# Kernel tuning notes

Measured on AMD Instinct MI355X. Metric: run time of the kernel, lower is better.

The kernel has to match this reference:

```python
import jax, jax.numpy as jnp
import numpy as np

HIDDEN = 128

def setup_inputs() -> dict:
    key = jax.random.key(0)
    ks = jax.random.split(key, 12)
    N, T, H = 4096, 64, HIDDEN
    s_in = 1.0 / np.sqrt(2.0)
    s_h = 1.0 / np.sqrt(H)
    return {
        "x_seq": jax.random.normal(ks[0], (N, T), dtype=jnp.float32),
        "m_seq": jax.random.uniform(ks[1], (N, T), dtype=jnp.float32),
        # linear layers stored as [in, out] (math identical to torch x @ W.T + b)
        "W_in": jax.random.normal(ks[2], (2, H), dtype=jnp.float32) * s_in,
        "b_in": jax.random.normal(ks[3], (H,), dtype=jnp.float32) * 0.01,
        "W_proj": jax.random.normal(ks[4], (H, H), dtype=jnp.float32) * s_h,
        "b_proj": jax.random.normal(ks[5], (H,), dtype=jnp.float32) * 0.01,
        "W_gcn": jax.random.normal(ks[6], (H, H), dtype=jnp.float32) * s_h,
        "b_gcn": jax.random.normal(ks[7], (H,), dtype=jnp.float32) * 0.01,
        "W_out": jax.random.normal(ks[8], (H, 1), dtype=jnp.float32) * s_h,
        "b_out": jax.random.normal(ks[9], (1,), dtype=jnp.float32) * 0.01,
    }


def reference(x_seq, m_seq, W_in, b_in, W_proj, b_proj, W_gcn, b_gcn, W_out, b_out):
    N, T = x_seq.shape
    H = W_in.shape[1]
    scale = 1.0 / jnp.sqrt(jnp.asarray(H, dtype=x_seq.dtype))
    # [T, N, 2] time-major inputs for scan
    xs = jnp.stack([x_seq, m_seq], axis=-1).transpose(1, 0, 2)
    h0 = jnp.zeros((N, H), dtype=x_seq.dtype)

    def step(h, inp_t):
        h_in = jax.nn.relu(inp_t @ W_in + b_in)            # [N, H]
        h_proj = h @ W_proj + b_proj                        # [N, H]
        A_dyn = jax.nn.softmax(h_proj @ h_proj.T * scale, axis=1)  # [N, N]
        msg = A_dyn @ h_in                                  # [N, H]
        h_new = jax.nn.relu(msg @ W_gcn + b_gcn + h_in)     # [N, H]
        pred = (h_new @ W_out + b_out)[:, 0]                # [N]
        return h_new, pred

    _, preds = jax.lax.scan(step, h0, xs)  # preds: [T, N]
    return preds.T  # [N, T]
```

## Files before the change

### kernel.cpp

```cpp
#include <hip/hip_runtime.h>
#include <math.h>

#define NN 4096
#define TT 64
#define HH 128
#define NNP 4160
#define SLICE (128 * NNP)
#define SPLITS 8
#define KPB (NN / SPLITS)
#define KT 32
#define NTILES (KPB / KT)
#define QB 64
#define SCALE 0.08838834764831845f
#define CSHIFT 16.0f

typedef __attribute__((ext_vector_type(8))) short short8;
typedef __attribute__((ext_vector_type(4))) float f32x4;
typedef unsigned long long u64;
#define MFMA(a, b, c)   __builtin_amdgcn_mfma_f32_16x16x32_bf16((a), (b), (c), 0, 0, 0)

__device__ __forceinline__ short f2b(float f) {
    union { float f; unsigned u; } v; v.f = f;
    unsigned r = v.u + 0x7fffu + ((v.u >> 16) & 1u);
    return (short)(r >> 16);
}
__device__ __forceinline__ float b2f(short s) {
    union { unsigned u; float f; } v; v.u = ((unsigned)(unsigned short)s) << 16;
    return v.f;
}
__device__ __forceinline__ void lds_fence() {
    __asm__ __volatile__("s_waitcnt lgkmcnt(0)" ::: "memory");
}


__global__ __launch_bounds__(256) void prep_kernel(
    const float* __restrict__ x_seq, const float* __restrict__ m_seq,
    const float* __restrict__ W_in,  const float* __restrict__ b_in,
    const float* __restrict__ W_proj,const float* __restrict__ b_proj,
    const float* __restrict__ W_gcn,
    short* __restrict__ hp, short* __restrict__ hinT_all,
    short* __restrict__ WgT, short* __restrict__ WpT)
{
    __shared__ __align__(16) short hb[128 * 66];
    const int b = blockIdx.x, tid = threadIdx.x;
    if (b < 256) {
        const int n0 = b * 16;
        for (int i = tid; i < 16 * HH; i += 256) {
            const int q = i >> 7, j = i & 127, n = n0 + q;
            hp[n * HH + j] = f2b(b_proj[j]);
        }
    } else if (b < 272) {
        const int wb = b - 256;
        #pragma unroll
        for (int k = 0; k < 4; ++k) {
            const int idx = wb * 1024 + k * 256 + tid;
            const int n = idx >> 7, kk = idx & 127;
            WgT[idx] = f2b(W_gcn[kk * HH + n]);
            WpT[idx] = f2b(W_proj[kk * HH + n]);
        }
    } else {
        const int u = b - 272;
        const int t = u >> 6, n0 = (u & 63) * 64;
        for (int i = tid; i < 64 * HH; i += 256) {
            const int q = i >> 7, j = i & 127, n = n0 + q;
            float hv = x_seq[n * TT + t] * W_in[j] + m_seq[n * TT + t] * W_in[HH + j] + b_in[j];
            hv = hv > 0.f ? hv : 0.f;
            hb[j * 66 + q] = f2b(hv);
        }
        __syncthreads();
        short* dst = hinT_all + (size_t)t * SLICE;
        for (int c = tid; c < 128 * 16; c += 256) {
            const int j = c >> 4, off = (c & 15) * 4;
            const int nb = n0 + off;
            const int tcol = (nb & ~31) | (((nb >> 2) & 3) << 3) | (((nb >> 4) & 1) << 2);
            const unsigned lo = *(const unsigned*)&hb[j * 66 + off];
            const unsigned hi = *(const unsigned*)&hb[j * 66 + off + 2];
            const u64 v = (u64)lo | ((u64)hi << 32);
            *(u64*)&dst[(size_t)j * NNP + tcol] = v;
        }
    }
}

__global__ __launch_bounds__(256, 3) void attn_kernel(
    const short* __restrict__ hp, const short* __restrict__ hinT,
    short* __restrict__ OpartB, float* __restrict__ lpart)
{
    __shared__ __align__(16) char pool[37888];
    short* KtS = (short*)pool;
    short* VtS = (short*)(pool + 17408);

    const int tid  = threadIdx.x;
    const int wave = tid >> 6, lane = tid & 63;
    const int ln = lane & 15, g = lane >> 4;
    const int split = blockIdx.x >> 6, qg = blockIdx.x & 63;
    const int q0 = qg * QB + wave * 16;
    const int kbase = split * KPB;

    const int krow = tid >> 4, kcol = (tid & 15) * 8;
    const int vrow = tid >> 2, vcol = (tid & 3) * 8;

    short8 qf[4];
    #pragma unroll
    for (int kc = 0; kc < 4; ++kc)
        qf[kc] = *(const short8*)&hp[(q0 + ln) * HH + kc * 32 + g * 8];

    f32x4 oacc[8] = {};
    f32x4 lacc = {};
    short8 vone;
    #pragma unroll
    for (int e = 0; e < 8; ++e) vone[e] = (short)0x3F80;

    short8 ksA0, ksA1, vsA0, vsA1;
    auto load_tile = [&](int kt_) {
        const int kb = kbase + kt_ * KT;
        ksA0 = *(const short8*)&hp  [(kb + krow) * HH + kcol];
        ksA1 = *(const short8*)&hp  [(kb + krow + 16) * HH + kcol];
        vsA0 = *(const short8*)&hinT[(size_t)vrow * NNP + kb + vcol];
        vsA1 = *(const short8*)&hinT[(size_t)(vrow + 64) * NNP + kb + vcol];
    };
    auto store_tile = [&](int b) {
        *(short8*)&KtS[b * 4352 + krow * 136 + kcol]        = ksA0;
        *(short8*)&KtS[b * 4352 + (krow + 16) * 136 + kcol] = ksA1;
        *(short8*)&VtS[b * 5120 + vrow * 40 + vcol]         = vsA0;
        *(short8*)&VtS[b * 5120 + (vrow + 64) * 40 + vcol]  = vsA1;
    };

    load_tile(0);
    store_tile(0);

    for (int kt = 0; kt < NTILES; ++kt) {
        const int b = kt & 1;
        __syncthreads();

        short8 kf[2][4], vf[8];
        #pragma unroll
        for (int kt2 = 0; kt2 < 2; ++kt2)
            #pragma unroll
            for (int kc = 0; kc < 4; ++kc)
                kf[kt2][kc] = *(const short8*)&KtS[b * 4352 + (kt2 * 16 + ln) * 136 + kc * 32 + g * 8];
        #pragma unroll
        for (int dt = 0; dt < 8; ++dt)
            vf[dt] = *(const short8*)&VtS[b * 5120 + (dt * 16 + ln) * 40 + g * 8];

        if (kt + 1 < NTILES) load_tile(kt + 1);

        f32x4 st[2] = {};
        __builtin_amdgcn_s_setprio(1);
        #pragma unroll
        for (int kt2 = 0; kt2 < 2; ++kt2)
            #pragma unroll
            for (int kc = 0; kc < 4; ++kc)
                st[kt2] = MFMA(kf[kt2][kc], qf[kc], st[kt2]);
        __builtin_amdgcn_s_setprio(0);

        short8 pa;
        #pragma unroll
        for (int e = 0; e < 8; ++e) {
            const float s = (e < 4) ? st[0][e] : st[1][e - 4];
            pa[e] = f2b(__expf(s * SCALE - CSHIFT));
        }

        if (kt + 1 < NTILES) store_tile(b ^ 1);

        __builtin_amdgcn_s_setprio(1);
        #pragma unroll
        for (int dt = 0; dt < 8; ++dt)
            oacc[dt] = MFMA(pa, vf[dt], oacc[dt]);
        lacc = MFMA(pa, vone, lacc);
        __builtin_amdgcn_s_setprio(0);
    }

    __syncthreads();

    if (ln == 0) {
        #pragma unroll
        for (int r = 0; r < 4; ++r)
            lpart[split * NN + q0 + g * 4 + r] = lacc[r];
    }

    short* bounce = (short*)pool + wave * 2048;
    #pragma unroll
    for (int dt = 0; dt < 8; ++dt)
        #pragma unroll
        for (int r = 0; r < 4; ++r)
            bounce[(g * 4 + r) * 128 + dt * 16 + ln] = f2b(oacc[dt][r]);
    lds_fence();
    #pragma unroll
    for (int sub = 0; sub < 4; ++sub) {
        const int qrow = sub * 4 + (lane >> 4), chunk = lane & 15;
        const short8 rd = *(const short8*)&bounce[qrow * 128 + chunk * 8];
        *(short8*)&OpartB[((size_t)split * NN + q0 + qrow) * HH + chunk * 8] = rd;
    }
}

__global__ __launch_bounds__(512) void fuse_kernel(
    const short* __restrict__ OpartB, const float* __restrict__ lpart,
    short* __restrict__ hp,
    const short* __restrict__ WgT, const short* __restrict__ WpT,
    const float* __restrict__ b_gcn, const float* __restrict__ b_proj,
    const float* __restrict__ W_out, const float* __restrict__ b_out,
    const float* __restrict__ x_seq, const float* __restrict__ m_seq,
    const float* __restrict__ W_in,  const float* __restrict__ b_in,
    float* __restrict__ out, int t)
{
    __shared__ __align__(16) short msgb[16 * 136];
    __shared__ __align__(16) short hnb[16 * 136];
    __shared__ float larr[16];
    __shared__ float ppd[8 * 16];

    const int tid = threadIdx.x;
    const int wave = tid >> 6, lane = tid & 63;
    const int ln = lane & 15, g = lane >> 4;
    const int fb = blockIdx.x;
    const int qg64 = (fb & 7) + 8 * (fb >> 5);
    const int qb = qg64 * 64 + ((fb >> 3) & 3) * 16;

    if (tid < 16) {
        float l = 0.f;
        #pragma unroll
        for (int sp = 0; sp < SPLITS; ++sp) l += lpart[sp * NN + qb + tid];
        larr[tid] = 1.0f / l;
    }
    __syncthreads();

    if (tid < 256) {
        const int q = tid >> 4, c8 = (tid & 15) * 8;
        float s[8] = {0.f, 0.f, 0.f, 0.f, 0.f, 0.f, 0.f, 0.f};
        #pragma unroll
        for (int sp = 0; sp < SPLITS; ++sp) {
            const short8 v = *(const short8*)&OpartB[((size_t)sp * NN + qb + q) * HH + c8];
            #pragma unroll
            for (int k = 0; k < 8; ++k) s[k] += b2f(v[k]);
        }
        const float inv = larr[q];
        short* mp = &msgb[q * 136 + c8];
        #pragma unroll
        for (int k = 0; k < 8; ++k) mp[k] = f2b(s[k] * inv);
    }
    __syncthreads();

    {
        short8 af[4];
        #pragma unroll
        for (int kc = 0; kc < 4; ++kc)
            af[kc] = *(const short8*)&msgb[ln * 136 + kc * 32 + g * 8];
        f32x4 c = {};
        #pragma unroll
        for (int kc = 0; kc < 4; ++kc)
            c = MFMA(af[kc], *(const short8*)&WgT[(wave * 16 + ln) * HH + kc * 32 + g * 8], c);
        const int j = wave * 16 + ln;
        const float bg = b_gcn[j], wo = W_out[j];
        const float wj0 = W_in[j], wj1 = W_in[HH + j], bj = b_in[j];
        float pr[4];
        #pragma unroll
        for (int r = 0; r < 4; ++r) {
            const int q = g * 4 + r;
            float hv = x_seq[(qb + q) * TT + t] * wj0 + m_seq[(qb + q) * TT + t] * wj1 + bj;
            hv = hv > 0.f ? hv : 0.f;
            float v = c[r] + bg + b2f(f2b(hv));
            v = v > 0.f ? v : 0.f;
            hnb[q * 136 + j] = f2b(v);
            pr[r] = v * wo;
        }
        #pragma unroll
        for (int r = 0; r < 4; ++r) {
            float p = pr[r];
            p += __shfl_xor(p, 1); p += __shfl_xor(p, 2);
            p += __shfl_xor(p, 4); p += __shfl_xor(p, 8);
            if (ln == 0) ppd[wave * 16 + g * 4 + r] = p;
        }
    }
    __syncthreads();

    if (tid < 16) {
        float s = b_out[0];
        #pragma unroll
        for (int w = 0; w < 8; ++w) s += ppd[w * 16 + tid];
        out[(qb + tid) * TT + t] = s;
    }

    if (t < TT - 1) {
        short8 hf[4];
        #pragma unroll
        for (int kc = 0; kc < 4; ++kc)
            hf[kc] = *(const short8*)&hnb[ln * 136 + kc * 32 + g * 8];
        f32x4 c = {};
        #pragma unroll
        for (int kc = 0; kc < 4; ++kc)
            c = MFMA(hf[kc], *(const short8*)&WpT[(wave * 16 + ln) * HH + kc * 32 + g * 8], c);
        const float bp = b_proj[wave * 16 + ln];
        #pragma unroll
        for (int r = 0; r < 4; ++r)
            hp[(qb + g * 4 + r) * HH + wave * 16 + ln] = f2b(c[r] + bp);
    }
}

extern "C" void kernel_launch(void* const* d_in, const int* in_sizes, int n_in,
                              void* d_out, int out_size, void* d_ws, size_t ws_size,
                              hipStream_t stream) {
    const float* x_seq  = (const float*)d_in[0];
    const float* m_seq  = (const float*)d_in[1];
    const float* W_in   = (const float*)d_in[2];
    const float* b_in   = (const float*)d_in[3];
    const float* W_proj = (const float*)d_in[4];
    const float* b_proj = (const float*)d_in[5];
    const float* W_gcn  = (const float*)d_in[6];
    const float* b_gcn  = (const float*)d_in[7];
    const float* W_out  = (const float*)d_in[8];
    const float* b_out  = (const float*)d_in[9];
    float* out = (float*)d_out;

    char* base = (char*)d_ws;
    const size_t MB = 1 << 20;
    short* hp       = (short*)(base + 0 * MB);
    short* WgT      = (short*)(base + 3 * MB);
    short* WpT      = (short*)(base + 3 * MB + 32768);
    float* lpart    = (float*)(base + 3 * MB + 65536);
    short* OpartB   = (short*)(base + 4 * MB);
    short* hinT_all = (short*)(base + 32 * MB);

    prep_kernel<<<272 + 64 * 64, 256, 0, stream>>>(x_seq, m_seq, W_in, b_in,
                                                   W_proj, b_proj, W_gcn,
                                                   hp, hinT_all, WgT, WpT);

    for (int t = 0; t < TT; ++t) {
        const short* hinT_t = hinT_all + (size_t)t * SLICE;
        attn_kernel<<<(NN / QB) * SPLITS, 256, 0, stream>>>(hp, hinT_t, OpartB, lpart);
        fuse_kernel<<<NN / 16, 512, 0, stream>>>(OpartB, lpart, hp,
                                                 WgT, WpT, b_gcn, b_proj, W_out, b_out,
                                                 x_seq, m_seq, W_in, b_in, out, t);
    }
}
```

Before: 1.613 ms.

## Give each attention wave two query tiles and split key tiles between wave pairs

Each wave in the attention kernel now covers 32 queries (two 16-row tiles) instead of 16, so every K/V fragment read from LDS feeds twice as many MFMAs. The block's key tiles are split in halves between the two wave pairs, and the partial outputs and row sums are merged through an fp32 LDS buffer before the bf16 write-out. The intent is to cut LDS fragment traffic per MFMA. In exchange, register pressure rises (launch bounds lowered to 2 blocks), half the waves sit idle in every key-tile iteration while still hitting the barriers, and the epilogue gains an extra cross-wave reduction.

```diff
diff --git a/kernel.cpp b/kernel.cpp
--- a/kernel.cpp
+++ b/kernel.cpp
@@ -81,31 +81,36 @@
     }
 }
 
-__global__ __launch_bounds__(256, 3) void attn_kernel(
+__global__ __launch_bounds__(256, 2) void attn_kernel(
     const short* __restrict__ hp, const short* __restrict__ hinT,
     short* __restrict__ OpartB, float* __restrict__ lpart)
 {
-    __shared__ __align__(16) char pool[37888];
+    __shared__ __align__(16) char pool[38144];
     short* KtS = (short*)pool;
     short* VtS = (short*)(pool + 17408);
+    float* obuf = (float*)pool;
+    float* lbuf = (float*)(pool + 33792);
 
     const int tid  = threadIdx.x;
     const int wave = tid >> 6, lane = tid & 63;
     const int ln = lane & 15, g = lane >> 4;
     const int split = blockIdx.x >> 6, qg = blockIdx.x & 63;
-    const int q0 = qg * QB + wave * 16;
+    const int qh = wave & 1, kh = wave >> 1;
+    const int q0 = qg * QB + qh * 32;
     const int kbase = split * KPB;
 
     const int krow = tid >> 4, kcol = (tid & 15) * 8;
     const int vrow = tid >> 2, vcol = (tid & 3) * 8;
 
-    short8 qf[4];
+    short8 qf[2][4];
     #pragma unroll
-    for (int kc = 0; kc < 4; ++kc)
-        qf[kc] = *(const short8*)&hp[(q0 + ln) * HH + kc * 32 + g * 8];
-
-    f32x4 oacc[8] = {};
-    f32x4 lacc = {};
+    for (int qt = 0; qt < 2; ++qt)
+        #pragma unroll
+        for (int kc = 0; kc < 4; ++kc)
+            qf[qt][kc] = *(const short8*)&hp[(q0 + qt * 16 + ln) * HH + kc * 32 + g * 8];
+
+    f32x4 oacc[2][8] = {};
+    f32x4 lacc[2] = {};
     short8 vone;
     #pragma unroll
     for (int e = 0; e < 8; ++e) vone[e] = (short)0x3F80;
@@ -132,64 +137,105 @@
         const int b = kt & 1;
         __syncthreads();
 
+        const bool act = ((kt >> 3) == kh);
         short8 kf[2][4], vf[8];
-        #pragma unroll
-        for (int kt2 = 0; kt2 < 2; ++kt2)
-            #pragma unroll
-            for (int kc = 0; kc < 4; ++kc)
-                kf[kt2][kc] = *(const short8*)&KtS[b * 4352 + (kt2 * 16 + ln) * 136 + kc * 32 + g * 8];
-        #pragma unroll
-        for (int dt = 0; dt < 8; ++dt)
-            vf[dt] = *(const short8*)&VtS[b * 5120 + (dt * 16 + ln) * 40 + g * 8];
+        if (act) {
+            #pragma unroll
+            for (int kt2 = 0; kt2 < 2; ++kt2)
+                #pragma unroll
+                for (int kc = 0; kc < 4; ++kc)
+                    kf[kt2][kc] = *(const short8*)&KtS[b * 4352 + (kt2 * 16 + ln) * 136 + kc * 32 + g * 8];
+            #pragma unroll
+            for (int dt = 0; dt < 8; ++dt)
+                vf[dt] = *(const short8*)&VtS[b * 5120 + (dt * 16 + ln) * 40 + g * 8];
+        }
 
         if (kt + 1 < NTILES) load_tile(kt + 1);
 
-        f32x4 st[2] = {};
-        __builtin_amdgcn_s_setprio(1);
-        #pragma unroll
-        for (int kt2 = 0; kt2 < 2; ++kt2)
-            #pragma unroll
-            for (int kc = 0; kc < 4; ++kc)
-                st[kt2] = MFMA(kf[kt2][kc], qf[kc], st[kt2]);
-        __builtin_amdgcn_s_setprio(0);
-
-        short8 pa;
-        #pragma unroll
-        for (int e = 0; e < 8; ++e) {
-            const float s = (e < 4) ? st[0][e] : st[1][e - 4];
-            pa[e] = f2b(__expf(s * SCALE - CSHIFT));
+        short8 pa[2];
+        if (act) {
+            f32x4 st[2][2] = {};
+            __builtin_amdgcn_s_setprio(1);
+            #pragma unroll
+            for (int kt2 = 0; kt2 < 2; ++kt2)
+                #pragma unroll
+                for (int qt = 0; qt < 2; ++qt)
+                    #pragma unroll
+                    for (int kc = 0; kc < 4; ++kc)
+                        st[kt2][qt] = MFMA(kf[kt2][kc], qf[qt][kc], st[kt2][qt]);
+            __builtin_amdgcn_s_setprio(0);
+
+            #pragma unroll
+            for (int qt = 0; qt < 2; ++qt) {
+                short8 paq;
+                #pragma unroll
+                for (int e = 0; e < 8; ++e) {
+                    const float s = (e < 4) ? st[0][qt][e] : st[1][qt][e - 4];
+                    paq[e] = f2b(__expf(s * SCALE - CSHIFT));
+                }
+                pa[qt] = paq;
+            }
         }
 
         if (kt + 1 < NTILES) store_tile(b ^ 1);
 
-        __builtin_amdgcn_s_setprio(1);
-        #pragma unroll
-        for (int dt = 0; dt < 8; ++dt)
-            oacc[dt] = MFMA(pa, vf[dt], oacc[dt]);
-        lacc = MFMA(pa, vone, lacc);
-        __builtin_amdgcn_s_setprio(0);
-    }
-
-    __syncthreads();
-
-    if (ln == 0) {
-        #pragma unroll
-        for (int r = 0; r < 4; ++r)
-            lpart[split * NN + q0 + g * 4 + r] = lacc[r];
-    }
-
-    short* bounce = (short*)pool + wave * 2048;
-    #pragma unroll
-    for (int dt = 0; dt < 8; ++dt)
-        #pragma unroll
-        for (int r = 0; r < 4; ++r)
-            bounce[(g * 4 + r) * 128 + dt * 16 + ln] = f2b(oacc[dt][r]);
-    lds_fence();
-    #pragma unroll
-    for (int sub = 0; sub < 4; ++sub) {
-        const int qrow = sub * 4 + (lane >> 4), chunk = lane & 15;
-        const short8 rd = *(const short8*)&bounce[qrow * 128 + chunk * 8];
-        *(short8*)&OpartB[((size_t)split * NN + q0 + qrow) * HH + chunk * 8] = rd;
+        if (act) {
+            __builtin_amdgcn_s_setprio(1);
+            #pragma unroll
+            for (int qt = 0; qt < 2; ++qt) {
+                #pragma unroll
+                for (int dt = 0; dt < 8; ++dt)
+                    oacc[qt][dt] = MFMA(pa[qt], vf[dt], oacc[qt][dt]);
+                lacc[qt] = MFMA(pa[qt], vone, lacc[qt]);
+            }
+            __builtin_amdgcn_s_setprio(0);
+        }
+    }
+
+    __syncthreads();
+
+    if (kh == 0) {
+        #pragma unroll
+        for (int qt = 0; qt < 2; ++qt) {
+            #pragma unroll
+            for (int dt = 0; dt < 8; ++dt)
+                #pragma unroll
+                for (int r = 0; r < 4; ++r)
+                    obuf[(qh * 32 + qt * 16 + g * 4 + r) * 132 + dt * 16 + ln] = oacc[qt][dt][r];
+            if (ln == 0) {
+                #pragma unroll
+                for (int r = 0; r < 4; ++r)
+                    lbuf[qh * 32 + qt * 16 + g * 4 + r] = lacc[qt][r];
+            }
+        }
+    }
+    __syncthreads();
+    if (kh == 1) {
+        #pragma unroll
+        for (int qt = 0; qt < 2; ++qt) {
+            #pragma unroll
+            for (int dt = 0; dt < 8; ++dt)
+                #pragma unroll
+                for (int r = 0; r < 4; ++r)
+                    obuf[(qh * 32 + qt * 16 + g * 4 + r) * 132 + dt * 16 + ln] += oacc[qt][dt][r];
+            if (ln == 0) {
+                #pragma unroll
+                for (int r = 0; r < 4; ++r) {
+                    const int row = qh * 32 + qt * 16 + g * 4 + r;
+                    lpart[split * NN + qg * QB + row] = lbuf[row] + lacc[qt][r];
+                }
+            }
+        }
+    }
+    __syncthreads();
+
+    for (int c = tid; c < QB * 16; c += 256) {
+        const int row = c >> 4, chunk = c & 15;
+        const float* src = &obuf[row * 132 + chunk * 8];
+        short8 rd;
+        #pragma unroll
+        for (int k = 0; k < 8; ++k) rd[k] = f2b(src[k]);
+        *(short8*)&OpartB[((size_t)split * NN + qg * QB + row) * HH + chunk * 8] = rd;
     }
 }
 
```

After: 1.789 ms. +10.9%, slower.
